# Performance work log

Measured on AMD Instinct MI355X. Metric: run time of the kernel, lower is better.

## Reference

```python
import jax, jax.numpy as jnp
import numpy as np
from jax import lax

EPS = 1e-5
D_CONV = 4
D_STATE = 8

def layer_norm(x, g, b):
    mu = x.mean(-1, keepdims=True)
    var = x.var(-1, keepdims=True)
    return (x - mu) * lax.rsqrt(var + EPS) * g + b

def causal_dw_conv(x, w, b):
    # x: [B, D, L], w: [D, K] depthwise causal conv, b: [D]
    K = w.shape[1]
    xp = jnp.pad(x, ((0, 0), (0, 0), (K - 1, 0)))
    out = lax.conv_general_dilated(
        xp, w[:, None, :], window_strides=(1,), padding='VALID',
        dimension_numbers=('NCH', 'OIH', 'NCH'), feature_group_count=w.shape[0])
    return out + b[None, :, None]

def mamba(x, in_w, conv_w, conv_b, xp_w, dt_w, dt_b, A_log, D, out_w):
    # x: [B, L, d_model]; faithful to mamba_ssm Mamba forward (selective_scan_ref math)
    Bb, L, _ = x.shape
    d_inner = in_w.shape[0] // 2
    dt_rank = dt_w.shape[1]
    xz = jnp.einsum('bld,ed->ble', x, in_w)
    xi, z = jnp.split(xz, 2, axis=-1)                      # [B,L,d_inner] each
    xc = causal_dw_conv(xi.swapaxes(1, 2), conv_w, conv_b).swapaxes(1, 2)
    xc = jax.nn.silu(xc)                                   # [B,L,d_inner]
    dbl = jnp.einsum('bld,ed->ble', xc, xp_w)
    dt, Bs, Cs = jnp.split(dbl, [dt_rank, dt_rank + D_STATE], axis=-1)
    delta = jax.nn.softplus(jnp.einsum('blr,dr->bld', dt, dt_w) + dt_b)
    A = -jnp.exp(A_log)                                    # [d_inner, d_state]
    dA = jnp.exp(delta[..., None] * A)                     # [B,L,D,S]
    dBx = delta[..., None] * Bs[:, :, None, :] * xc[..., None]
    def step(h, inp):
        dA_t, dBx_t, c_t = inp
        h = dA_t * h + dBx_t                               # [B,D,S]
        return h, jnp.einsum('bds,bs->bd', h, c_t)
    h0 = jnp.zeros((Bb, d_inner, D_STATE), x.dtype)
    _, ys = lax.scan(step, h0, (dA.swapaxes(0, 1), dBx.swapaxes(0, 1), Cs.swapaxes(0, 1)))
    y = ys.swapaxes(0, 1) + xc * D                         # [B,L,D]
    y = y * jax.nn.silu(z)
    return jnp.einsum('bld,od->blo', y, out_w)

def setup_inputs() -> dict:
    key = jax.random.key(0)
    ks = jax.random.split(key, 4)
    B, C, H = 2, 128, 16
    L = H * H * H
    def nrm(k, shape, s=0.02):
        return jax.random.normal(k, shape, jnp.float32) * s
    inp = {}
    inp['x'] = jax.random.normal(ks[0], (B, C, H, H, H), jnp.float32)
    inp['ln1_g'] = jnp.ones((C,), jnp.float32)
    inp['ln1_b'] = jnp.zeros((C,), jnp.float32)
    inp['ln2_g'] = jnp.ones((L,), jnp.float32)
    inp['ln2_b'] = jnp.zeros((L,), jnp.float32)
    def mamba_params(kbase, d_model):
        d_inner = 2 * d_model
        dt_rank = d_model // 16
        kk = jax.random.split(kbase, 6)
        return {
            'in_w': nrm(kk[0], (2 * d_inner, d_model)),
            'conv_w': nrm(kk[1], (d_inner, D_CONV), 0.3),
            'conv_b': jnp.zeros((d_inner,), jnp.float32),
            'xp_w': nrm(kk[2], (dt_rank + 2 * D_STATE, d_inner)),
            'dt_w': nrm(kk[3], (d_inner, dt_rank), 0.1),
            'dt_b': jax.random.uniform(kk[4], (d_inner,), jnp.float32, -4.6, -2.3),
            'Alog': jnp.broadcast_to(jnp.log(jnp.arange(1, D_STATE + 1, dtype=jnp.float32)), (d_inner, D_STATE)) + jnp.zeros((d_inner, D_STATE), jnp.float32),
            'D': jnp.ones((d_inner,), jnp.float32),
            'out_w': nrm(kk[5], (d_model, d_inner)),
        }
    for pfx, dm, k in (('m1_', C, ks[1]), ('m2_', L, ks[2])):
        for name, v in mamba_params(k, dm).items():
            inp[pfx + name] = v
    return inp

def reference(x, ln1_g, ln1_b, ln2_g, ln2_b,
              m1_in_w, m1_conv_w, m1_conv_b, m1_xp_w, m1_dt_w, m1_dt_b, m1_Alog, m1_D, m1_out_w,
              m2_in_w, m2_conv_w, m2_conv_b, m2_xp_w, m2_dt_w, m2_dt_b, m2_Alog, m2_D, m2_out_w):
    B, C = x.shape[:2]
    xf = x.reshape(B, C, -1)          # [B, n_tokens, L]
    xc = xf.swapaxes(1, 2)            # [B, L, n_tokens]
    yc = mamba(layer_norm(xc, ln1_g, ln1_b),
               m1_in_w, m1_conv_w, m1_conv_b, m1_xp_w, m1_dt_w, m1_dt_b,
               m1_Alog, m1_D, m1_out_w).swapaxes(1, 2)
    ys = mamba(layer_norm(xf, ln2_g, ln2_b),
               m2_in_w, m2_conv_w, m2_conv_b, m2_xp_w, m2_dt_w, m2_dt_b,
               m2_Alog, m2_D, m2_out_w)
    # dropout is identity in eval mode
    return (yc + ys + xf).reshape(x.shape)
```

## Files before the change

kernel.cpp:

```cpp
#include <hip/hip_runtime.h>
#include <math.h>

typedef __attribute__((ext_vector_type(8))) short s16x8;
typedef __attribute__((ext_vector_type(4))) short s16x4;
typedef __attribute__((ext_vector_type(4))) float f32x4;

#define DEVINL __device__ __forceinline__

DEVINL short f2bf(float f) {
    unsigned u = __float_as_uint(f);
    u += 0x7fffu + ((u >> 16) & 1u);
    return (short)(u >> 16);
}
DEVINL float softplusf(float x) { return (x > 20.f) ? x : log1pf(expf(x)); }
DEVINL float siluf(float z) { return z / (1.f + expf(-z)); }

typedef __attribute__((address_space(1))) const unsigned GblU32;
typedef __attribute__((address_space(3))) unsigned LdsU32;
DEVINL void gload_lds16(const void* g, void* l) {
    __builtin_amdgcn_global_load_lds((GblU32*)g, (LdsU32*)l, 16, 0, 0);
}

__global__ __launch_bounds__(256) void ln1_kernel(const float* __restrict__ x,
    const float* __restrict__ g, const float* __restrict__ bb, short* __restrict__ out)
{
    __shared__ float tile[64 * 129];
    int b = blockIdx.x >> 6;
    int l0 = (blockIdx.x & 63) << 6;
    int t = threadIdx.x;
    int ll = t & 63, c0 = t >> 6;
    for (int c = c0; c < 128; c += 4)
        tile[ll * 129 + c] = x[((size_t)(b * 128 + c) << 12) + l0 + ll];
    __syncthreads();
    int r = t >> 2, q = t & 3;
    float s1 = 0.f, s2 = 0.f;
    #pragma unroll 8
    for (int j = 0; j < 32; ++j) {
        float v = tile[r * 129 + q * 32 + j];
        s1 += v; s2 += v * v;
    }
    s1 += __shfl_xor(s1, 1); s2 += __shfl_xor(s2, 1);
    s1 += __shfl_xor(s1, 2); s2 += __shfl_xor(s2, 2);
    float mean = s1 * (1.f / 128.f);
    float var  = s2 * (1.f / 128.f) - mean * mean;
    float rstd = rsqrtf(var + 1e-5f);
    short* orow = out + ((size_t)((b << 12) + l0 + r) << 7);
    for (int j = 0; j < 32; j += 4) {
        int c = q * 32 + j;
        s16x4 pk;
        #pragma unroll
        for (int i = 0; i < 4; ++i)
            pk[i] = f2bf((tile[r * 129 + c + i] - mean) * rstd * g[c + i] + bb[c + i]);
        *(s16x4*)&orow[c] = pk;
    }
}

__global__ __launch_bounds__(256) void ln2_kernel(const float* __restrict__ x,
    const float* __restrict__ g, const float* __restrict__ bb, short* __restrict__ out)
{
    int m = blockIdx.x, t = threadIdx.x;
    const float* row = x + (size_t)m * 4096;
    f32x4 vals[4];
    float s1 = 0.f, s2 = 0.f;
    #pragma unroll
    for (int j = 0; j < 4; ++j) {
        vals[j] = *(const f32x4*)(row + j * 1024 + t * 4);
        #pragma unroll
        for (int i = 0; i < 4; ++i) { s1 += vals[j][i]; s2 += vals[j][i] * vals[j][i]; }
    }
    #pragma unroll
    for (int off = 32; off; off >>= 1) { s1 += __shfl_xor(s1, off); s2 += __shfl_xor(s2, off); }
    __shared__ float red[8];
    int wv = t >> 6;
    if ((t & 63) == 0) { red[wv] = s1; red[4 + wv] = s2; }
    __syncthreads();
    s1 = red[0] + red[1] + red[2] + red[3];
    s2 = red[4] + red[5] + red[6] + red[7];
    float mean = s1 * (1.f / 4096.f);
    float var  = s2 * (1.f / 4096.f) - mean * mean;
    float rstd = rsqrtf(var + 1e-5f);
    short* orow = out + (size_t)m * 4096;
    #pragma unroll
    for (int j = 0; j < 4; ++j) {
        int idx = j * 1024 + t * 4;
        f32x4 gv = *(const f32x4*)(g + idx);
        f32x4 bv = *(const f32x4*)(bb + idx);
        s16x4 pk;
        #pragma unroll
        for (int i = 0; i < 4; ++i)
            pk[i] = f2bf((vals[j][i] - mean) * rstd * gv[i] + bv[i]);
        *(s16x4*)&orow[idx] = pk;
    }
}

template<int BM, int BN, int WM, int WN, int EPI>
__global__ __launch_bounds__(256) void gemm_bt(
    const short* __restrict__ A, const float* __restrict__ W,
    float* __restrict__ C, const float* __restrict__ bias,
    int M, int Nreal, int K, int kLen, int ldc)
{
    constexpr int FM = BM / (WM * 16);
    constexpr int FN = BN / (WN * 16);
    constexpr int NISSA = BM / 32;
    constexpr int NW = (BN * 16) / 256;
    __shared__ short Al[2][BM * 64];
    __shared__ short Wl[2][BN * 64];
    const int tid = threadIdx.x;
    const int lane = tid & 63;
    const int wv = tid >> 6;
    const int lr = lane & 15, kh = lane >> 4;
    const int wm = wv % WM, wn = wv / WM;
    const int n0 = blockIdx.x * BN;
    const int m0 = blockIdx.y * BM;
    const int k0 = blockIdx.z * kLen;
    const int nt = kLen >> 6;
    const int srcSlot = (lane & 7) ^ (lane >> 3);

    f32x4 acc[FM][FN];
    #pragma unroll
    for (int a = 0; a < FM; ++a)
        #pragma unroll
        for (int b = 0; b < FN; ++b) acc[a][b] = (f32x4){0.f, 0.f, 0.f, 0.f};
    f32x4 wreg[NW];

    auto stageA = [&](int buf, int kg) {
        #pragma unroll
        for (int i = 0; i < NISSA; ++i) {
            int c = wv * NISSA + i;
            int r = c * 8 + (lane >> 3);
            const short* src = A + (size_t)(m0 + r) * K + kg + srcSlot * 8;
            gload_lds16(src, &Al[buf][c * 512]);
        }
    };
    auto loadW = [&](int kg) {
        #pragma unroll
        for (int j = 0; j < NW; ++j) {
            int idx = j * 256 + tid;
            int row = idx >> 4, q = idx & 15;
            int gn = n0 + row;
            if (gn < Nreal) wreg[j] = *(const f32x4*)(W + (size_t)gn * K + kg + q * 4);
            else            wreg[j] = (f32x4){0.f, 0.f, 0.f, 0.f};
        }
    };
    auto writeW = [&](int buf) {
        #pragma unroll
        for (int j = 0; j < NW; ++j) {
            int idx = j * 256 + tid;
            int row = idx >> 4, q = idx & 15;
            s16x4 pk;
            #pragma unroll
            for (int i = 0; i < 4; ++i) pk[i] = f2bf(wreg[j][i]);
            int byte = row * 128 + (((q >> 1) ^ (row & 7)) << 4) + ((q & 1) << 3);
            *(s16x4*)((char*)&Wl[buf][0] + byte) = pk;
        }
    };
    auto compute = [&](int buf) {
        #pragma unroll
        for (int ks = 0; ks < 2; ++ks) {
            s16x8 af[FM], bfr[FN];
            #pragma unroll
            for (int mi = 0; mi < FM; ++mi) {
                int r = wm * (BM / WM) + mi * 16 + lr;
                int byte = r * 128 + (((ks * 4 + kh) ^ (r & 7)) << 4);
                af[mi] = *(const s16x8*)((const char*)&Al[buf][0] + byte);
            }
            #pragma unroll
            for (int ni = 0; ni < FN; ++ni) {
                int w = wn * (BN / WN) + ni * 16 + lr;
                int byte = w * 128 + (((ks * 4 + kh) ^ (w & 7)) << 4);
                bfr[ni] = *(const s16x8*)((const char*)&Wl[buf][0] + byte);
            }
            #pragma unroll
            for (int mi = 0; mi < FM; ++mi)
                #pragma unroll
                for (int ni = 0; ni < FN; ++ni)
                    acc[mi][ni] = __builtin_amdgcn_mfma_f32_16x16x32_bf16(
                        af[mi], bfr[ni], acc[mi][ni], 0, 0, 0);
        }
    };

    loadW(k0);
    stageA(0, k0);
    writeW(0);
    __syncthreads();

    int cur = 0;
    for (int t = 0; t < nt; ++t) {
        const int kn = k0 + (t + 1) * 64;
        if (t + 1 < nt) { loadW(kn); stageA(cur ^ 1, kn); }
        compute(cur);
        if (t + 1 < nt) writeW(cur ^ 1);
        __syncthreads();
        cur ^= 1;
    }

    float* Cz = C + (size_t)blockIdx.z * M * ldc;
    #pragma unroll
    for (int mi = 0; mi < FM; ++mi) {
        #pragma unroll
        for (int ni = 0; ni < FN; ++ni) {
            int gn = n0 + wn * (BN / WN) + ni * 16 + lr;
            if (gn < Nreal) {
                #pragma unroll
                for (int j = 0; j < 4; ++j) {
                    int gm = m0 + wm * (BM / WM) + mi * 16 + kh * 4 + j;
                    float v = acc[mi][ni][j];
                    if constexpr (EPI == 1) v = softplusf(v + bias[gn]);
                    Cz[(size_t)gm * ldc + gn] = v;
                }
            }
        }
    }
}

__global__ __launch_bounds__(256) void conv1_kernel(const float* __restrict__ xz,
    const float* __restrict__ cw, const float* __restrict__ cb,
    float* __restrict__ xcf, short* __restrict__ xcb)
{
    int idx = blockIdx.x * 256 + threadIdx.x;
    int d = idx & 255;
    int l = (idx >> 8) & 4095;
    int b = idx >> 20;
    f32x4 wv = *(const f32x4*)(cw + d * 4);
    float acc = cb[d];
    #pragma unroll
    for (int j = 0; j < 4; ++j) {
        int ll = l - 3 + j;
        if (ll >= 0) acc += xz[((size_t)((b << 12) + ll) << 9) + d] * wv[j];
    }
    acc = siluf(acc);
    size_t o = ((size_t)((b << 12) + l) << 8) + d;
    xcf[o] = acc;
    xcb[o] = f2bf(acc);
}

__global__ __launch_bounds__(256) void conv2_kernel(const float* __restrict__ xz,
    const float* __restrict__ cw, const float* __restrict__ cb,
    float* __restrict__ xcf, short* __restrict__ xcb)
{
    int idx = blockIdx.x * 256 + threadIdx.x;
    int d = idx & 8191;
    int t = (idx >> 13) & 127;
    int b = idx >> 20;
    f32x4 wv = *(const f32x4*)(cw + d * 4);
    float acc = cb[d];
    #pragma unroll
    for (int j = 0; j < 4; ++j) {
        int tt = t - 3 + j;
        if (tt >= 0) acc += xz[((size_t)((b << 7) + tt) << 14) + d] * wv[j];
    }
    acc = siluf(acc);
    size_t o = ((size_t)((b << 7) + t) << 13) + d;
    xcf[o] = acc;
    xcb[o] = f2bf(acc);
}

__global__ __launch_bounds__(256) void dtproj1_kernel(const float* __restrict__ dbl,
    const float* __restrict__ dtw, const float* __restrict__ dtb, float* __restrict__ delta)
{
    int m = blockIdx.x;
    int d = threadIdx.x;
    const float* dtv = dbl + (size_t)m * 32;
    f32x4 w0 = *(const f32x4*)(dtw + d * 8);
    f32x4 w1 = *(const f32x4*)(dtw + d * 8 + 4);
    float acc = dtb[d];
    #pragma unroll
    for (int j = 0; j < 4; ++j) acc += dtv[j] * w0[j];
    #pragma unroll
    for (int j = 0; j < 4; ++j) acc += dtv[4 + j] * w1[j];
    delta[(size_t)m * 256 + d] = softplusf(acc);
}

__global__ __launch_bounds__(256) void scan1_p1(const float* __restrict__ delta,
    const float* __restrict__ xc, const float* __restrict__ dbl,
    const float* __restrict__ alog, float* __restrict__ hch, float* __restrict__ pch)
{
    int b = blockIdx.x >> 7, ch = blockIdx.x & 127;
    int d = threadIdx.x;
    __shared__ float bc[512];
    for (int i = threadIdx.x; i < 512; i += 256) {
        int j = i >> 4, s = i & 15;
        bc[i] = dbl[(size_t)((b << 12) + (ch << 5) + j) * 32 + 8 + s];
    }
    float a[8], h[8], P[8];
    #pragma unroll
    for (int s = 0; s < 8; ++s) { a[s] = -expf(alog[d * 8 + s]); h[s] = 0.f; P[s] = 1.f; }
    __syncthreads();
    for (int j = 0; j < 32; ++j) {
        size_t row = (b << 12) + (ch << 5) + j;
        float dl = delta[(row << 8) + d];
        float xv = xc[(row << 8) + d];
        float dx = dl * xv;
        #pragma unroll
        for (int s = 0; s < 8; ++s) {
            float dA = expf(dl * a[s]);
            h[s] = dA * h[s] + dx * bc[(j << 4) + s];
            P[s] *= dA;
        }
    }
    size_t base = (((size_t)((b << 7) + ch) << 8) + d) << 3;
    #pragma unroll
    for (int s = 0; s < 8; ++s) { hch[base + s] = h[s]; pch[base + s] = P[s]; }
}

__global__ __launch_bounds__(256) void scan1_p2(const float* __restrict__ hch,
    const float* __restrict__ pch, float* __restrict__ hin)
{
    int b = blockIdx.x >> 3;
    int idx = ((blockIdx.x & 7) << 8) + threadIdx.x;
    float h = 0.f;
    size_t o0 = (((size_t)(b << 7)) << 11) + idx;
    float pc = pch[o0], hc = hch[o0];
    for (int c = 0; c < 128; ++c) {
        size_t o = (((size_t)((b << 7) + c)) << 11) + idx;
        float pn = 0.f, hn = 0.f;
        if (c < 127) { pn = pch[o + 2048]; hn = hch[o + 2048]; }
        hin[o] = h;
        h = pc * h + hc;
        pc = pn; hc = hn;
    }
}

__global__ __launch_bounds__(256) void scan1_p3(const float* __restrict__ delta,
    const float* __restrict__ xc, const float* __restrict__ dbl,
    const float* __restrict__ alog, const float* __restrict__ hin,
    const float* __restrict__ Dw, const float* __restrict__ xz,
    short* __restrict__ ybf)
{
    int b = blockIdx.x >> 7, ch = blockIdx.x & 127;
    int d = threadIdx.x;
    __shared__ float bc[512];
    for (int i = threadIdx.x; i < 512; i += 256) {
        int j = i >> 4, s = i & 15;
        bc[i] = dbl[(size_t)((b << 12) + (ch << 5) + j) * 32 + 8 + s];
    }
    float a[8], h[8];
    size_t base = (((size_t)((b << 7) + ch) << 8) + d) << 3;
    #pragma unroll
    for (int s = 0; s < 8; ++s) { a[s] = -expf(alog[d * 8 + s]); h[s] = hin[base + s]; }
    float Dv = Dw[d];
    __syncthreads();
    for (int j = 0; j < 32; ++j) {
        size_t row = (b << 12) + (ch << 5) + j;
        float dl = delta[(row << 8) + d];
        float xv = xc[(row << 8) + d];
        float dx = dl * xv;
        float y = 0.f;
        #pragma unroll
        for (int s = 0; s < 8; ++s) {
            float dA = expf(dl * a[s]);
            h[s] = dA * h[s] + dx * bc[(j << 4) + s];
            y += h[s] * bc[(j << 4) + 8 + s];
        }
        float z = xz[(row << 9) + 256 + d];
        ybf[(row << 8) + d] = f2bf((y + xv * Dv) * siluf(z));
    }
}

__global__ void xp2_finish(const float* __restrict__ part, short* __restrict__ dtb,
                           float* __restrict__ Bs, float* __restrict__ Cs)
{
    int m = blockIdx.x, t = threadIdx.x;
    if (t >= 272) return;
    float s = 0.f;
    #pragma unroll
    for (int p = 0; p < 32; ++p) s += part[(size_t)p * 73728 + m * 288 + t];
    if (t < 256)       dtb[m * 256 + t] = f2bf(s);
    else if (t < 264)  Bs[m * 8 + t - 256] = s;
    else               Cs[m * 8 + t - 264] = s;
}

__global__ __launch_bounds__(64) void scan2_kernel(const float* __restrict__ delta,
    const float* __restrict__ xc, const float* __restrict__ Bs,
    const float* __restrict__ Cs, const float* __restrict__ xz,
    const float* __restrict__ alog, const float* __restrict__ Dw,
    short* __restrict__ ybf)
{
    int b = blockIdx.x >> 7;
    int d = ((blockIdx.x & 127) << 6) + threadIdx.x;
    __shared__ float bc[2048];
    for (int i = threadIdx.x; i < 2048; i += 64) {
        int t = i >> 4, s = i & 15;
        bc[i] = (s < 8) ? Bs[((b << 7) + t) * 8 + s] : Cs[((b << 7) + t) * 8 + s - 8];
    }
    float a[8], h[8];
    #pragma unroll
    for (int s = 0; s < 8; ++s) { a[s] = -expf(alog[(size_t)d * 8 + s]); h[s] = 0.f; }
    float Dv = Dw[d];
    __syncthreads();
    for (int t = 0; t < 128; ++t) {
        size_t row = (b << 7) + t;
        float dl = delta[(row << 13) + d];
        float xv = xc[(row << 13) + d];
        float dx = dl * xv;
        float y = 0.f;
        #pragma unroll
        for (int s = 0; s < 8; ++s) {
            float dA = expf(dl * a[s]);
            h[s] = dA * h[s] + dx * bc[(t << 4) + s];
            y += h[s] * bc[(t << 4) + 8 + s];
        }
        float z = xz[(row << 14) + 8192 + d];
        ybf[(row << 13) + d] = f2bf((y + xv * Dv) * siluf(z));
    }
}

__global__ __launch_bounds__(256) void final_kernel(const float* __restrict__ x,
    const float* __restrict__ y1out, const float* __restrict__ part2,
    float* __restrict__ out)
{
    __shared__ float tl[64 * 65];
    int bz = blockIdx.x;
    int b = bz >> 7, rem = bz & 127;
    int c0 = (rem >> 6) << 6, l0 = (rem & 63) << 6;
    int t = threadIdx.x;
    int lrow = t >> 4, cq = (t & 15) << 2;
    #pragma unroll
    for (int jj = 0; jj < 4; ++jj) {
        int l = l0 + lrow + jj * 16;
        f32x4 v = *(const f32x4*)&y1out[((size_t)((b << 12) + l) << 7) + c0 + cq];
        #pragma unroll
        for (int i = 0; i < 4; ++i) tl[(cq + i) * 65 + lrow + jj * 16] = v[i];
    }
    __syncthreads();
    int lc = t & 63, cr = t >> 6;
    for (int j = 0; j < 16; ++j) {
        int cl = j * 4 + cr;
        size_t addr = ((size_t)((b << 7) + c0 + cl) << 12) + l0 + lc;
        float v = x[addr] + tl[cl * 65 + lc];
        v += part2[addr] + part2[1048576 + addr] + part2[2 * 1048576 + addr] + part2[3 * 1048576 + addr];
        out[addr] = v;
    }
}

extern "C" void kernel_launch(void* const* d_in, const int* in_sizes, int n_in,
                              void* d_out, int out_size, void* d_ws, size_t ws_size,
                              hipStream_t stream)
{
    (void)in_sizes; (void)n_in; (void)out_size; (void)ws_size;
    const float* x        = (const float*)d_in[0];
    const float* ln1_g    = (const float*)d_in[1];
    const float* ln1_b    = (const float*)d_in[2];
    const float* ln2_g    = (const float*)d_in[3];
    const float* ln2_b    = (const float*)d_in[4];
    const float* m1_in_w  = (const float*)d_in[5];
    const float* m1_cw    = (const float*)d_in[6];
    const float* m1_cb    = (const float*)d_in[7];
    const float* m1_xp_w  = (const float*)d_in[8];
    const float* m1_dt_w  = (const float*)d_in[9];
    const float* m1_dt_b  = (const float*)d_in[10];
    const float* m1_Alog  = (const float*)d_in[11];
    const float* m1_D     = (const float*)d_in[12];
    const float* m1_out_w = (const float*)d_in[13];
    const float* m2_in_w  = (const float*)d_in[14];
    const float* m2_cw    = (const float*)d_in[15];
    const float* m2_cb    = (const float*)d_in[16];
    const float* m2_xp_w  = (const float*)d_in[17];
    const float* m2_dt_w  = (const float*)d_in[18];
    const float* m2_dt_b  = (const float*)d_in[19];
    const float* m2_Alog  = (const float*)d_in[20];
    const float* m2_D     = (const float*)d_in[21];
    const float* m2_out_w = (const float*)d_in[22];
    float* out = (float*)d_out;

    char* wsp = (char*)d_ws;
    size_t off = 0;
    auto alloc = [&](size_t bytes) -> void* {
        void* p = wsp + off;
        off += (bytes + 255) & ~(size_t)255;
        return p;
    };

    float* y1out = (float*)alloc((size_t)8192 * 128 * 4);
    size_t off0 = off;

    short* xln1   = (short*)alloc((size_t)8192 * 128 * 2);
    float* xz1    = (float*)alloc((size_t)8192 * 512 * 4);
    float* xc1f   = (float*)alloc((size_t)8192 * 256 * 4);
    short* xc1b   = (short*)alloc((size_t)8192 * 256 * 2);
    float* dbl1   = (float*)alloc((size_t)8192 * 32 * 4);
    float* delta1 = (float*)alloc((size_t)8192 * 256 * 4);
    float* hch    = (float*)alloc((size_t)256 * 2048 * 4);
    float* pch    = (float*)alloc((size_t)256 * 2048 * 4);
    float* hin    = (float*)alloc((size_t)256 * 2048 * 4);
    short* y1b    = (short*)alloc((size_t)8192 * 256 * 2);

    ln1_kernel<<<128, 256, 0, stream>>>(x, ln1_g, ln1_b, xln1);
    gemm_bt<128, 64, 2, 2, 0><<<dim3(8, 64, 1), 256, 0, stream>>>(xln1, m1_in_w, xz1, nullptr, 8192, 512, 128, 128, 512);
    conv1_kernel<<<8192, 256, 0, stream>>>(xz1, m1_cw, m1_cb, xc1f, xc1b);
    gemm_bt<128, 32, 2, 2, 0><<<dim3(1, 64, 1), 256, 0, stream>>>(xc1b, m1_xp_w, dbl1, nullptr, 8192, 24, 256, 256, 32);
    dtproj1_kernel<<<8192, 256, 0, stream>>>(dbl1, m1_dt_w, m1_dt_b, delta1);
    scan1_p1<<<256, 256, 0, stream>>>(delta1, xc1f, dbl1, m1_Alog, hch, pch);
    scan1_p2<<<16, 256, 0, stream>>>(hch, pch, hin);
    scan1_p3<<<256, 256, 0, stream>>>(delta1, xc1f, dbl1, m1_Alog, hin, m1_D, xz1, y1b);
    gemm_bt<128, 64, 2, 2, 0><<<dim3(2, 64, 1), 256, 0, stream>>>(y1b, m1_out_w, y1out, nullptr, 8192, 128, 256, 256, 128);

    off = off0;
    short* xln2   = (short*)alloc((size_t)256 * 4096 * 2);
    float* xz2    = (float*)alloc((size_t)256 * 16384 * 4);
    float* xc2f   = (float*)alloc((size_t)256 * 8192 * 4);
    short* xc2b   = (short*)alloc((size_t)256 * 8192 * 2);
    float* xp2p   = (float*)alloc((size_t)32 * 256 * 288 * 4);
    short* dt2b   = (short*)alloc((size_t)256 * 256 * 2);
    float* Bs2    = (float*)alloc((size_t)256 * 8 * 4);
    float* Cs2    = (float*)alloc((size_t)256 * 8 * 4);
    float* delta2 = (float*)alloc((size_t)256 * 8192 * 4);
    short* y2b    = (short*)alloc((size_t)256 * 8192 * 2);
    float* out2p  = (float*)alloc((size_t)4 * 256 * 4096 * 4);

    ln2_kernel<<<256, 256, 0, stream>>>(x, ln2_g, ln2_b, xln2);
    gemm_bt<256, 64, 4, 1, 0><<<dim3(256, 1, 1), 256, 0, stream>>>(xln2, m2_in_w, xz2, nullptr, 256, 16384, 4096, 4096, 16384);
    conv2_kernel<<<8192, 256, 0, stream>>>(xz2, m2_cw, m2_cb, xc2f, xc2b);
    gemm_bt<256, 64, 4, 1, 0><<<dim3(5, 1, 32), 256, 0, stream>>>(xc2b, m2_xp_w, xp2p, nullptr, 256, 272, 8192, 256, 288);
    xp2_finish<<<256, 288, 0, stream>>>(xp2p, dt2b, Bs2, Cs2);
    gemm_bt<256, 64, 4, 1, 1><<<dim3(128, 1, 1), 256, 0, stream>>>(dt2b, m2_dt_w, delta2, m2_dt_b, 256, 8192, 256, 256, 8192);
    scan2_kernel<<<256, 64, 0, stream>>>(delta2, xc2f, Bs2, Cs2, xz2, m2_Alog, m2_D, y2b);
    gemm_bt<256, 64, 4, 1, 0><<<dim3(64, 1, 4), 256, 0, stream>>>(y2b, m2_out_w, out2p, nullptr, 256, 4096, 8192, 2048, 4096);
    final_kernel<<<256, 256, 0, stream>>>(x, y1out, out2p, out);
}
```

Measured before the change: 831.9 us.

## Split-K the mamba2 GEMMs and reduce partials in consumers; prefetch scan inputs

The in_proj, dt_proj and out_proj GEMMs of the second mamba now use split-K over the grid z dimension to put more blocks on the GPU. The partial sums are added in the consumers: the conv kernel sums the two in_proj halves, the scan kernel sums the dt halves and the z halves and applies bias plus softplus itself, and the final kernel sums eight out_proj partials. The scan kernels also register-prefetch the next four timesteps to hide global load latency. In exchange, partial buffers and redundant reads grow, since z partials are re-read and the final kernel reads twice as much data.

Result: no change. 847.5 us (+1.9%).

```diff
diff --git a/kernel.cpp b/kernel.cpp
--- a/kernel.cpp
+++ b/kernel.cpp
@@ -234,7 +234,7 @@
     xcb[o] = f2bf(acc);
 }
 
-__global__ __launch_bounds__(256) void conv2_kernel(const float* __restrict__ xz,
+__global__ __launch_bounds__(256) void conv2r_kernel(const float* __restrict__ p,
     const float* __restrict__ cw, const float* __restrict__ cb,
     float* __restrict__ xcf, short* __restrict__ xcb)
 {
@@ -247,7 +247,10 @@
     #pragma unroll
     for (int j = 0; j < 4; ++j) {
         int tt = t - 3 + j;
-        if (tt >= 0) acc += xz[((size_t)((b << 7) + tt) << 14) + d] * wv[j];
+        if (tt >= 0) {
+            size_t a = ((size_t)((b << 7) + tt) << 14) + d;
+            acc += (p[a] + p[4194304 + a]) * wv[j];
+        }
     }
     acc = siluf(acc);
     size_t o = ((size_t)((b << 7) + t) << 13) + d;
@@ -308,16 +311,24 @@
 {
     int b = blockIdx.x >> 3;
     int idx = ((blockIdx.x & 7) << 8) + threadIdx.x;
+    float pc[4], hc[4];
+    #pragma unroll
+    for (int i = 0; i < 4; ++i) {
+        size_t o = (((size_t)((b << 7) + i)) << 11) + idx;
+        pc[i] = pch[o]; hc[i] = hch[o];
+    }
     float h = 0.f;
-    size_t o0 = (((size_t)(b << 7)) << 11) + idx;
-    float pc = pch[o0], hc = hch[o0];
+    #pragma unroll 4
     for (int c = 0; c < 128; ++c) {
+        int s = c & 3;
         size_t o = (((size_t)((b << 7) + c)) << 11) + idx;
-        float pn = 0.f, hn = 0.f;
-        if (c < 127) { pn = pch[o + 2048]; hn = hch[o + 2048]; }
+        float pv = pc[s], hv = hc[s];
+        if (c + 4 < 128) {
+            size_t o4 = o + (4ull << 11);
+            pc[s] = pch[o4]; hc[s] = hch[o4];
+        }
         hin[o] = h;
-        h = pc * h + hc;
-        pc = pn; hc = hn;
+        h = pv * h + hv;
     }
 }
 
@@ -370,11 +381,11 @@
     else               Cs[m * 8 + t - 264] = s;
 }
 
-__global__ __launch_bounds__(64) void scan2_kernel(const float* __restrict__ delta,
+__global__ __launch_bounds__(64) void scan2_kernel(const float* __restrict__ dp,
     const float* __restrict__ xc, const float* __restrict__ Bs,
-    const float* __restrict__ Cs, const float* __restrict__ xz,
-    const float* __restrict__ alog, const float* __restrict__ Dw,
-    short* __restrict__ ybf)
+    const float* __restrict__ Cs, const float* __restrict__ zp,
+    const float* __restrict__ dtb, const float* __restrict__ alog,
+    const float* __restrict__ Dw, short* __restrict__ ybf)
 {
     int b = blockIdx.x >> 7;
     int d = ((blockIdx.x & 127) << 6) + threadIdx.x;
@@ -387,11 +398,30 @@
     #pragma unroll
     for (int s = 0; s < 8; ++s) { a[s] = -expf(alog[(size_t)d * 8 + s]); h[s] = 0.f; }
     float Dv = Dw[d];
-    __syncthreads();
+    float bias = dtb[d];
+    float pd0[4], pd1[4], px[4], pz0[4], pz1[4];
+    #pragma unroll
+    for (int i = 0; i < 4; ++i) {
+        size_t rD = ((size_t)((b << 7) + i) << 13) + d;
+        size_t rZ = ((size_t)((b << 7) + i) << 14) + 8192 + d;
+        pd0[i] = dp[rD]; pd1[i] = dp[2097152 + rD];
+        px[i]  = xc[rD];
+        pz0[i] = zp[rZ]; pz1[i] = zp[4194304 + rZ];
+    }
+    __syncthreads();
+    #pragma unroll 4
     for (int t = 0; t < 128; ++t) {
-        size_t row = (b << 7) + t;
-        float dl = delta[(row << 13) + d];
-        float xv = xc[(row << 13) + d];
+        int s4 = t & 3;
+        float dl = softplusf(pd0[s4] + pd1[s4] + bias);
+        float xv = px[s4];
+        float zz = pz0[s4] + pz1[s4];
+        if (t + 4 < 128) {
+            size_t rD = ((size_t)((b << 7) + t + 4) << 13) + d;
+            size_t rZ = ((size_t)((b << 7) + t + 4) << 14) + 8192 + d;
+            pd0[s4] = dp[rD]; pd1[s4] = dp[2097152 + rD];
+            px[s4]  = xc[rD];
+            pz0[s4] = zp[rZ]; pz1[s4] = zp[4194304 + rZ];
+        }
         float dx = dl * xv;
         float y = 0.f;
         #pragma unroll
@@ -400,8 +430,8 @@
             h[s] = dA * h[s] + dx * bc[(t << 4) + s];
             y += h[s] * bc[(t << 4) + 8 + s];
         }
-        float z = xz[(row << 14) + 8192 + d];
-        ybf[(row << 13) + d] = f2bf((y + xv * Dv) * siluf(z));
+        size_t row = (b << 7) + t;
+        ybf[(row << 13) + d] = f2bf((y + xv * Dv) * siluf(zz));
     }
 }
 
@@ -428,7 +458,8 @@
         int cl = j * 4 + cr;
         size_t addr = ((size_t)((b << 7) + c0 + cl) << 12) + l0 + lc;
         float v = x[addr] + tl[cl * 65 + lc];
-        v += part2[addr] + part2[1048576 + addr] + part2[2 * 1048576 + addr] + part2[3 * 1048576 + addr];
+        #pragma unroll
+        for (int p = 0; p < 8; ++p) v += part2[(size_t)p * 1048576 + addr];
         out[addr] = v;
     }
 }
@@ -497,24 +528,24 @@
 
     off = off0;
     short* xln2   = (short*)alloc((size_t)256 * 4096 * 2);
-    float* xz2    = (float*)alloc((size_t)256 * 16384 * 4);
+    float* xz2p   = (float*)alloc((size_t)2 * 256 * 16384 * 4);
     float* xc2f   = (float*)alloc((size_t)256 * 8192 * 4);
     short* xc2b   = (short*)alloc((size_t)256 * 8192 * 2);
     float* xp2p   = (float*)alloc((size_t)32 * 256 * 288 * 4);
     short* dt2b   = (short*)alloc((size_t)256 * 256 * 2);
     float* Bs2    = (float*)alloc((size_t)256 * 8 * 4);
     float* Cs2    = (float*)alloc((size_t)256 * 8 * 4);
-    float* delta2 = (float*)alloc((size_t)256 * 8192 * 4);
+    float* delta2p= (float*)alloc((size_t)2 * 256 * 8192 * 4);
     short* y2b    = (short*)alloc((size_t)256 * 8192 * 2);
-    float* out2p  = (float*)alloc((size_t)4 * 256 * 4096 * 4);
+    float* out2p  = (float*)alloc((size_t)8 * 256 * 4096 * 4);
 
     ln2_kernel<<<256, 256, 0, stream>>>(x, ln2_g, ln2_b, xln2);
-    gemm_bt<256, 64, 4, 1, 0><<<dim3(256, 1, 1), 256, 0, stream>>>(xln2, m2_in_w, xz2, nullptr, 256, 16384, 4096, 4096, 16384);
-    conv2_kernel<<<8192, 256, 0, stream>>>(xz2, m2_cw, m2_cb, xc2f, xc2b);
+    gemm_bt<256, 64, 4, 1, 0><<<dim3(256, 1, 2), 256, 0, stream>>>(xln2, m2_in_w, xz2p, nullptr, 256, 16384, 4096, 2048, 16384);
+    conv2r_kernel<<<8192, 256, 0, stream>>>(xz2p, m2_cw, m2_cb, xc2f, xc2b);
     gemm_bt<256, 64, 4, 1, 0><<<dim3(5, 1, 32), 256, 0, stream>>>(xc2b, m2_xp_w, xp2p, nullptr, 256, 272, 8192, 256, 288);
     xp2_finish<<<256, 288, 0, stream>>>(xp2p, dt2b, Bs2, Cs2);
-    gemm_bt<256, 64, 4, 1, 1><<<dim3(128, 1, 1), 256, 0, stream>>>(dt2b, m2_dt_w, delta2, m2_dt_b, 256, 8192, 256, 256, 8192);
-    scan2_kernel<<<256, 64, 0, stream>>>(delta2, xc2f, Bs2, Cs2, xz2, m2_Alog, m2_D, y2b);
-    gemm_bt<256, 64, 4, 1, 0><<<dim3(64, 1, 4), 256, 0, stream>>>(y2b, m2_out_w, out2p, nullptr, 256, 4096, 8192, 2048, 4096);
+    gemm_bt<256, 64, 4, 1, 0><<<dim3(128, 1, 2), 256, 0, stream>>>(dt2b, m2_dt_w, delta2p, nullptr, 256, 8192, 256, 128, 8192);
+    scan2_kernel<<<256, 64, 0, stream>>>(delta2p, xc2f, Bs2, Cs2, xz2p, m2_dt_b, m2_Alog, m2_D, y2b);
+    gemm_bt<256, 64, 4, 1, 0><<<dim3(64, 1, 8), 256, 0, stream>>>(y2b, m2_out_w, out2p, nullptr, 256, 4096, 8192, 1024, 4096);
     final_kernel<<<256, 256, 0, stream>>>(x, y1out, out2p, out);
 }
```
